# Optimization experiments

Hardware: AMD Instinct MI355X
Metric: run time of the kernel (lower is better)

The kernel has to match this reference:

```python
import jax, jax.numpy as jnp
import numpy as np

B, T, F = 64, 512, 256
ENC = 256      # encoder output dim
P = 128        # projection_dim
H = 256        # gru_hidden_dim
K = 12         # num_future_steps
TEMP = 0.1


def setup_inputs() -> dict:
    key = jax.random.key(0)
    ks = jax.random.split(key, 12)
    s = lambda *d: 1.0 / np.sqrt(d[0])
    return {
        "x_seq": jax.random.normal(ks[0], (B, T, F), jnp.float32),
        # encoder: Dense(F -> ENC)
        "W_enc": jax.random.normal(ks[1], (F, ENC), jnp.float32) * s(F),
        "b_enc": jnp.zeros((ENC,), jnp.float32),
        # projection: Dense(ENC -> P)
        "W_proj": jax.random.normal(ks[2], (ENC, P), jnp.float32) * s(ENC),
        "b_proj": jnp.zeros((P,), jnp.float32),
        # GRUCell (flax convention: input dense has bias, hidden dense bias only on n)
        "Wi": jax.random.normal(ks[3], (P, 3 * H), jnp.float32) * s(P),
        "bi": jnp.zeros((3 * H,), jnp.float32),
        "Wh": jax.random.normal(ks[4], (H, 3 * H), jnp.float32) * s(H),
        "bhn": jnp.zeros((H,), jnp.float32),
        # K predictors: Dense(H -> P)
        "Wp": jax.random.normal(ks[5], (K, H, P), jnp.float32) * s(H),
        "bp": jnp.zeros((K, P), jnp.float32),
    }


def _gru_scan(z_seq, Wi, bi, Wh, bhn):
    # z_seq: [B, T, P] -> c_seq: [B, T, H]
    def step(h, x_t):
        gi = x_t @ Wi + bi          # [B, 3H]
        gh = h @ Wh                 # [B, 3H]
        ir, iz, inn = jnp.split(gi, 3, axis=-1)
        hr, hz, hn = jnp.split(gh, 3, axis=-1)
        r = jax.nn.sigmoid(ir + hr)
        z = jax.nn.sigmoid(iz + hz)
        n = jnp.tanh(inn + r * (hn + bhn))
        h_new = (1.0 - z) * n + z * h
        return h_new, h_new

    h0 = jnp.zeros((z_seq.shape[0], Wh.shape[0]), z_seq.dtype)
    _, c = jax.lax.scan(step, h0, jnp.swapaxes(z_seq, 0, 1))  # c: [T, B, H]
    return jnp.swapaxes(c, 0, 1)


def reference(x_seq, W_enc, b_enc, W_proj, b_proj, Wi, bi, Wh, bhn, Wp, bp):
    # encoder per timestep (vmap(vmap(Dense)) == batched matmul)
    z_seq = x_seq @ W_enc + b_enc                 # [B, T, ENC]
    z_seq = z_seq @ W_proj + b_proj               # [B, T, P]
    c_seq = _gru_scan(z_seq, Wi, bi, Wh, bhn)     # [B, T, H]

    Tlen = z_seq.shape[1]
    loss = jnp.asarray(0.0, z_seq.dtype)
    for k in range(1, K + 1):
        if Tlen - k <= 0:
            continue
        z_pos = z_seq[:, k:]                      # [B, T-k, P]
        pred = c_seq[:, :-k] @ Wp[k - 1] + bp[k - 1]  # [B, T-k, P]
        logits = jnp.einsum('btd,bkd->btk', pred, z_pos) / TEMP
        labels = jnp.arange(logits.shape[1])
        # NOTE: faithful to source: [..., labels] with labels=arange is an
        # identity gather along the last axis (not a diagonal pick).
        loss = loss + jnp.mean(-jax.nn.log_softmax(logits, axis=-1)[..., labels])
    return loss / K
```

## Files before the change

kernel.cpp:

```cpp
#include <hip/hip_runtime.h>
#include <hip/hip_bf16.h>
#include <math.h>

#define B_   64
#define T_   512
#define F_   256
#define ENC_ 256
#define P_   128
#define H_   256
#define K_   12
#define INV_TEMP 10.0f

typedef unsigned short u16;
typedef _Float16 half2v __attribute__((ext_vector_type(2)));
union U2H { unsigned int u; half2v h; };
typedef __attribute__((ext_vector_type(8))) short bf16x8;
typedef __attribute__((ext_vector_type(4))) float f32x4;
typedef _Float16 f16x8 __attribute__((ext_vector_type(8)));
union BF8 { bf16x8 v; u16 e[8]; };

__device__ __forceinline__ float rcpf(float x) {
#if __has_builtin(__builtin_amdgcn_rcpf)
    return __builtin_amdgcn_rcpf(x);
#else
    return 1.f / x;
#endif
}
__device__ __forceinline__ u16 f2bf(float f) {
    unsigned int u = __float_as_uint(f);
    unsigned int r = (u + 0x7fffu + ((u >> 16) & 1u)) >> 16;
    return (u16)r;
}
__device__ __forceinline__ float bf2f(u16 v) {
    return __uint_as_float(((unsigned int)v) << 16);
}
__device__ __forceinline__ float bflo(unsigned int u) { return __uint_as_float(u << 16); }
__device__ __forceinline__ float bfhi(unsigned int u) { return __uint_as_float(u & 0xffff0000u); }
__device__ __forceinline__ float wave_sum(float v) {
    #pragma unroll
    for (int o = 32; o > 0; o >>= 1) v += __shfl_down(v, o, 64);
    return v;
}

__global__ __launch_bounds__(256) void setup_conv(const float* __restrict__ Wh,
                                                  _Float16* __restrict__ Wht,
                                                  const float* __restrict__ Wi,
                                                  u16* __restrict__ Wit,
                                                  const float* __restrict__ Wp,
                                                  u16* __restrict__ Wpt,
                                                  const float* __restrict__ We,
                                                  const float* __restrict__ be,
                                                  const float* __restrict__ Wpj,
                                                  const float* __restrict__ bpj,
                                                  u16* __restrict__ Wct,
                                                  float* __restrict__ bc,
                                                  float* __restrict__ accum) {
    int bid = blockIdx.x;
    if (bid < 192) {
        __shared__ float tile0[32][33];
        int g0 = (bid % 24) * 32, k0 = (bid / 24) * 32;
        int tx = threadIdx.x & 31, ty = threadIdx.x >> 5;
        #pragma unroll
        for (int i = 0; i < 32; i += 8)
            tile0[ty + i][tx] = Wh[(size_t)(k0 + ty + i) * 768 + g0 + tx];
        __syncthreads();
        #pragma unroll
        for (int i = 0; i < 32; i += 8)
            Wht[(size_t)(g0 + ty + i) * 256 + k0 + tx] = (_Float16)tile0[tx][ty + i];
    } else if (bid < 288) {
        __shared__ float tile[32][33];
        int b2 = bid - 192;
        int n0 = (b2 % 24) * 32, k0 = (b2 / 24) * 32;
        int tx = threadIdx.x & 31, ty = threadIdx.x >> 5;
        #pragma unroll
        for (int i = 0; i < 32; i += 8)
            tile[ty + i][tx] = Wi[(size_t)(k0 + ty + i) * 768 + n0 + tx];
        __syncthreads();
        #pragma unroll
        for (int i = 0; i < 32; i += 8)
            Wit[(size_t)(n0 + ty + i) * 128 + k0 + tx] = f2bf(tile[tx][ty + i]);
    } else if (bid < 672) {
        __shared__ float tile2[32][33];
        int b3 = bid - 288;
        int kq = b3 / 32, rem = b3 % 32;
        int h0 = (rem % 8) * 32, p0 = (rem / 8) * 32;
        int tx = threadIdx.x & 31, ty = threadIdx.x >> 5;
        #pragma unroll
        for (int i = 0; i < 32; i += 8)
            tile2[ty + i][tx] = Wp[(size_t)kq * H_ * P_ + (size_t)(h0 + ty + i) * P_ + p0 + tx];
        __syncthreads();
        #pragma unroll
        for (int i = 0; i < 32; i += 8)
            Wpt[(size_t)kq * P_ * H_ + (size_t)(p0 + ty + i) * H_ + h0 + tx] = f2bf(tile2[tx][ty + i]);
    } else {
        int f = (bid - 672) * 2 + (threadIdx.x >> 7);
        int p = threadIdx.x & 127;
        if (f < F_) {
            float a = 0.f;
            for (int e = 0; e < ENC_; e++) a = fmaf(We[f * ENC_ + e], Wpj[e * P_ + p], a);
            Wct[(size_t)p * F_ + f] = f2bf(a);
        } else if (f == F_) {
            float a = bpj[p];
            for (int e = 0; e < ENC_; e++) a = fmaf(be[e], Wpj[e * P_ + p], a);
            bc[p] = a;
        } else {
            #pragma unroll
            for (int i = 0; i < 8; i++) accum[p * 8 + i] = 0.f;
        }
    }
}

__global__ __launch_bounds__(256) void gemm_mfma_f32a(const float* __restrict__ A,
                                                      const u16* __restrict__ Bt,
                                                      const float* __restrict__ bias,
                                                      u16* __restrict__ Ch,
                                                      int N, int K) {
    int tid  = threadIdx.x;
    int w    = tid >> 6;
    int lane = tid & 63;
    int col  = lane & 15;
    int quad = lane >> 4;
    int bm = blockIdx.y * 64, bn = blockIdx.x * 128;

    f32x4 acc[8] = {};
    const float* arow = A + (size_t)(bm + w * 16 + col) * K;
    #pragma unroll
    for (int k0 = 0; k0 < K; k0 += 32) {
        float4 v0 = *(const float4*)(arow + k0 + quad * 8);
        float4 v1 = *(const float4*)(arow + k0 + quad * 8 + 4);
        BF8 af;
        af.e[0] = f2bf(v0.x); af.e[1] = f2bf(v0.y); af.e[2] = f2bf(v0.z); af.e[3] = f2bf(v0.w);
        af.e[4] = f2bf(v1.x); af.e[5] = f2bf(v1.y); af.e[6] = f2bf(v1.z); af.e[7] = f2bf(v1.w);
        #pragma unroll
        for (int nt = 0; nt < 8; nt++) {
            bf16x8 bf = *(const bf16x8*)(Bt + (size_t)(bn + nt * 16 + col) * K + k0 + quad * 8);
            acc[nt] = __builtin_amdgcn_mfma_f32_16x16x32_bf16(af.v, bf, acc[nt], 0, 0, 0);
        }
    }
    #pragma unroll
    for (int nt = 0; nt < 8; nt++) {
        int gn = bn + nt * 16 + col;
        float bv = bias[gn];
        #pragma unroll
        for (int r = 0; r < 4; r++) {
            int gm = bm + w * 16 + quad * 4 + r;
            Ch[(size_t)gm * N + gn] = f2bf(acc[nt][r] + bv);
        }
    }
}

__global__ __launch_bounds__(256) void gemm_mfma(const u16* __restrict__ A,
                                                 const u16* __restrict__ Bt,
                                                 const float* __restrict__ bias,
                                                 u16* __restrict__ Ch,
                                                 int N, int K) {
    int tid  = threadIdx.x;
    int w    = tid >> 6;
    int lane = tid & 63;
    int col  = lane & 15;
    int quad = lane >> 4;
    int bm = blockIdx.y * 64, bn = blockIdx.x * 128;

    f32x4 acc[8] = {};
    const u16* arow = A + (size_t)(bm + w * 16 + col) * K;
    #pragma unroll
    for (int k0 = 0; k0 < K; k0 += 32) {
        bf16x8 af = *(const bf16x8*)(arow + k0 + quad * 8);
        #pragma unroll
        for (int nt = 0; nt < 8; nt++) {
            bf16x8 bf = *(const bf16x8*)(Bt + (size_t)(bn + nt * 16 + col) * K + k0 + quad * 8);
            acc[nt] = __builtin_amdgcn_mfma_f32_16x16x32_bf16(af, bf, acc[nt], 0, 0, 0);
        }
    }
    #pragma unroll
    for (int nt = 0; nt < 8; nt++) {
        int gn = bn + nt * 16 + col;
        float bv = bias[gn];
        #pragma unroll
        for (int r = 0; r < 4; r++) {
            int gm = bm + w * 16 + quad * 4 + r;
            Ch[(size_t)gm * N + gn] = f2bf(acc[nt][r] + bv);
        }
    }
}

#define GRUB_ 64

__global__ __attribute__((amdgpu_flat_work_group_size(512, 512)))
void gru_zsum_kernel(const u16* __restrict__ gi,
                     const _Float16* __restrict__ Wht,
                     const float* __restrict__ bhn,
                     u16* __restrict__ ch,
                     const u16* __restrict__ zh,
                     float* __restrict__ zsum) {
    __shared__ __align__(16) char smem[8704];
    int tid = threadIdx.x;

    if (blockIdx.x >= GRUB_) {
        float (*part)[128] = (float (*)[128])smem;
        int b   = blockIdx.x - GRUB_;
        int pg  = tid & 31;
        int g   = tid >> 5;
        const u16* zb = zh + (size_t)b * T_ * P_;
        float s0 = 0.f, s1 = 0.f, s2 = 0.f, s3 = 0.f;
        for (int t = 1 + g; t < T_; t += 16) {
            uint2 v = *(const uint2*)(zb + (size_t)t * P_ + pg * 4);
            s0 += bflo(v.x); s1 += bfhi(v.x);
            s2 += bflo(v.y); s3 += bfhi(v.y);
        }
        part[g][pg * 4 + 0] = s0; part[g][pg * 4 + 1] = s1;
        part[g][pg * 4 + 2] = s2; part[g][pg * 4 + 3] = s3;
        __syncthreads();
        if (tid < 128) {
            float s = 0.f;
            #pragma unroll
            for (int g2 = 0; g2 < 16; g2++) s += part[g2][tid];
            zsum[(size_t)b * P_ + tid] = s;
        }
        return;
    }

    _Float16* hbase = (_Float16*)smem;

    int lane = tid & 63, w = tid >> 6;
    int col  = lane & 15, quad = lane >> 4;
    int b    = blockIdx.x;
    int jj0  = w * 32 + col;

    f16x8 wf[3][2][8];
    #pragma unroll
    for (int g = 0; g < 3; g++)
        #pragma unroll
        for (int n2 = 0; n2 < 2; n2++) {
            const _Float16* src = Wht + (size_t)(g * 256 + jj0 + n2 * 16) * 256 + quad * 8;
            #pragma unroll
            for (int k0 = 0; k0 < 8; k0++)
                wf[g][n2][k0] = *(const f16x8*)(src + k0 * 32);
        }
    #pragma unroll
    for (int g = 0; g < 3; g++)
        #pragma unroll
        for (int n2 = 0; n2 < 2; n2++)
            #pragma unroll
            for (int k0 = 0; k0 < 8; k0++)
                asm volatile("" : "+v"(wf[g][n2][k0]));

    for (int i = tid; i < 528; i += 512) hbase[i] = (_Float16)0.f;

    const u16* gb = gi + (size_t)b * T_ * 768;
    u16* cb       = ch + (size_t)b * T_ * 256;
    float bh0 = bhn[jj0], bh1 = bhn[jj0 + 16];
    float hold0 = 0.f, hold1 = 0.f;
    unsigned int pf[2][6];

    {
        pf[0][0] = gb[jj0];        pf[0][1] = gb[jj0 + 16];
        pf[0][2] = gb[256 + jj0];  pf[0][3] = gb[256 + jj0 + 16];
        pf[0][4] = gb[512 + jj0];  pf[0][5] = gb[512 + jj0 + 16];
    }
    __syncthreads();

    auto body = [&](int t, int c, int pt) {
        int n = c ^ 1;
        if (pt < T_) {
            const u16* gr = gb + (size_t)pt * 768;
            pf[n][0] = gr[jj0];        pf[n][1] = gr[jj0 + 16];
            pf[n][2] = gr[256 + jj0];  pf[n][3] = gr[256 + jj0 + 16];
            pf[n][4] = gr[512 + jj0];  pf[n][5] = gr[512 + jj0 + 16];
        }
        const _Float16* HC = hbase + c * 264;
        _Float16*       HN = hbase + n * 264;
        f32x4 aR0 = {}, aR1 = {}, aZ0 = {}, aZ1 = {}, aN0 = {}, aN1 = {};
        #pragma unroll
        for (int k0 = 0; k0 < 8; k0++) {
            f16x8 af = *(const f16x8*)(HC + k0 * 32 + quad * 8);
            aR0 = __builtin_amdgcn_mfma_f32_16x16x32_f16(af, wf[0][0][k0], aR0, 0, 0, 0);
            aR1 = __builtin_amdgcn_mfma_f32_16x16x32_f16(af, wf[0][1][k0], aR1, 0, 0, 0);
            aZ0 = __builtin_amdgcn_mfma_f32_16x16x32_f16(af, wf[1][0][k0], aZ0, 0, 0, 0);
            aZ1 = __builtin_amdgcn_mfma_f32_16x16x32_f16(af, wf[1][1][k0], aZ1, 0, 0, 0);
            aN0 = __builtin_amdgcn_mfma_f32_16x16x32_f16(af, wf[2][0][k0], aN0, 0, 0, 0);
            aN1 = __builtin_amdgcn_mfma_f32_16x16x32_f16(af, wf[2][1][k0], aN1, 0, 0, 0);
        }
        float rg0 = rcpf(1.f + __expf(-(bf2f((u16)pf[c][0]) + aR0[0])));
        float rg1 = rcpf(1.f + __expf(-(bf2f((u16)pf[c][1]) + aR1[0])));
        float zg0 = rcpf(1.f + __expf(-(bf2f((u16)pf[c][2]) + aZ0[0])));
        float zg1 = rcpf(1.f + __expf(-(bf2f((u16)pf[c][3]) + aZ1[0])));
        float xn0 = bf2f((u16)pf[c][4]) + rg0 * (aN0[0] + bh0);
        float xn1 = bf2f((u16)pf[c][5]) + rg1 * (aN1[0] + bh1);
        float nn0 = fmaf(2.f, rcpf(1.f + __expf(-2.f * xn0)), -1.f);
        float nn1 = fmaf(2.f, rcpf(1.f + __expf(-2.f * xn1)), -1.f);
        hold0 = (1.f - zg0) * nn0 + zg0 * hold0;
        hold1 = (1.f - zg1) * nn1 + zg1 * hold1;
        if (quad == 0) {
            HN[jj0]      = (_Float16)hold0;
            HN[jj0 + 16] = (_Float16)hold1;
        } else if (quad == 1) {
            u16* cr = cb + (size_t)t * 256;
            cr[jj0]      = f2bf(hold0);
            cr[jj0 + 16] = f2bf(hold1);
        }
        asm volatile("s_waitcnt lgkmcnt(0)" ::: "memory");
        __builtin_amdgcn_s_barrier();
        asm volatile("" ::: "memory");
    };

    #pragma unroll 1
    for (int t = 0; t < T_; t += 2) {
        body(t,     0, t + 1);
        body(t + 1, 1, t + 2);
    }
}

__global__ __launch_bounds__(512) void loss_fused(const u16* __restrict__ ch,
                                                  const u16* __restrict__ Wpt,
                                                  const float* __restrict__ bp,
                                                  const u16* __restrict__ zh,
                                                  const float* __restrict__ zsum,
                                                  float* __restrict__ accum) {
    __shared__ u16 Pst[128][136];
    __shared__ u16 Zt[64][136];
    __shared__ float sS[128];
    __shared__ float red[8];
    int k  = blockIdx.z + 1;
    int b  = blockIdx.y;
    int t0 = blockIdx.x * 128;
    int Tk = T_ - k;
    int tid  = threadIdx.x;
    int w    = tid >> 6;
    int lane = tid & 63;
    int col  = lane & 15;
    int quad = lane >> 4;
    const u16* zb = zh + (size_t)b * T_ * P_;

    if (tid < 128) {
        float s = zsum[(size_t)b * P_ + tid];
        for (int t = 1; t < k; t++) s -= bf2f(zb[(size_t)t * P_ + tid]);
        sS[tid] = s;
    }

    {
        f32x4 acc[8] = {};
        const u16* arow = ch + ((size_t)b * T_ + t0 + w * 16 + col) * H_;
        const u16* wk   = Wpt + (size_t)(k - 1) * P_ * H_;
        #pragma unroll
        for (int k0 = 0; k0 < 8; k0++) {
            bf16x8 af = *(const bf16x8*)(arow + k0 * 32 + quad * 8);
            #pragma unroll
            for (int nt = 0; nt < 8; nt++) {
                bf16x8 bf = *(const bf16x8*)(wk + (size_t)(nt * 16 + col) * H_ + k0 * 32 + quad * 8);
                acc[nt] = __builtin_amdgcn_mfma_f32_16x16x32_bf16(af, bf, acc[nt], 0, 0, 0);
            }
        }
        #pragma unroll
        for (int nt = 0; nt < 8; nt++) {
            float bias = bp[(size_t)(k - 1) * P_ + nt * 16 + col];
            #pragma unroll
            for (int r = 0; r < 4; r++)
                Pst[w * 16 + quad * 4 + r][nt * 16 + col] = f2bf(acc[nt][r] + bias);
        }
    }
    __syncthreads();

    float mloc[4], sloc[4];
    #pragma unroll
    for (int r = 0; r < 4; r++) { mloc[r] = -INFINITY; sloc[r] = 0.f; }

    for (int ct = 0; ct < Tk; ct += 64) {
        __syncthreads();
        {
            int cc = tid;
            #pragma unroll
            for (int rep = 0; rep < 2; rep++, cc += 512) {
                int row = cc >> 4;
                int off = (cc & 15) * 8;
                int tcol = k + ct + row;
                *(uint4*)&Zt[row][off] = *(const uint4*)(zb + (size_t)tcol * P_ + off);
            }
        }
        __syncthreads();
        f32x4 acc[4] = {};
        #pragma unroll
        for (int k0 = 0; k0 < 4; k0++) {
            bf16x8 af = *(const bf16x8*)(&Pst[w * 16 + col][k0 * 32 + quad * 8]);
            #pragma unroll
            for (int nt = 0; nt < 4; nt++) {
                bf16x8 bf = *(const bf16x8*)(&Zt[nt * 16 + col][k0 * 32 + quad * 8]);
                acc[nt] = __builtin_amdgcn_mfma_f32_16x16x32_bf16(af, bf, acc[nt], 0, 0, 0);
            }
        }
        #pragma unroll
        for (int r = 0; r < 4; r++) {
            float l[4];
            float tmax = -INFINITY;
            #pragma unroll
            for (int nt = 0; nt < 4; nt++) {
                bool valid = (ct + nt * 16 + col) < Tk;
                l[nt] = valid ? acc[nt][r] * INV_TEMP : -INFINITY;
                tmax = fmaxf(tmax, l[nt]);
            }
            float mnew = fmaxf(mloc[r], tmax);
            float e = __expf(l[0] - mnew) + __expf(l[1] - mnew)
                    + __expf(l[2] - mnew) + __expf(l[3] - mnew);
            sloc[r] = sloc[r] * __expf(mloc[r] - mnew) + e;
            mloc[r] = mnew;
        }
    }
    #pragma unroll
    for (int r = 0; r < 4; r++) {
        #pragma unroll
        for (int o = 1; o < 16; o <<= 1) {
            float mo = __shfl_xor(mloc[r], o, 64);
            float so = __shfl_xor(sloc[r], o, 64);
            float mn = fmaxf(mloc[r], mo);
            sloc[r] = sloc[r] * __expf(mloc[r] - mn) + so * __expf(mo - mn);
            mloc[r] = mn;
        }
    }
    float tkinv = INV_TEMP / (float)Tk;
    float scale = 1.0f / ((float)K_ * (float)B_ * (float)Tk);
    float bs = 0.f;
    #pragma unroll
    for (int r = 0; r < 4; r++) {
        int row = w * 16 + quad * 4 + r;
        BF8 pv;
        pv.v = *(const bf16x8*)(&Pst[row][col * 8]);
        float d = 0.f;
        #pragma unroll
        for (int m = 0; m < 8; m++) d = fmaf(bf2f(pv.e[m]), sS[col * 8 + m], d);
        #pragma unroll
        for (int o = 1; o < 16; o <<= 1) d += __shfl_xor(d, o, 64);
        int gr = t0 + row;
        if (gr < Tk) bs += mloc[r] + __logf(sloc[r]) - d * tkinv;
    }
    if (col != 0) bs = 0.f;
    bs = wave_sum(bs);
    if (lane == 0) red[w] = bs;
    __syncthreads();
    if (tid == 0) {
        float tot = 0.f;
        #pragma unroll
        for (int i = 0; i < 8; i++) tot += red[i];
        atomicAdd(&accum[(blockIdx.x * 809 + b * 67 + blockIdx.z * 131) & 1023],
                  tot * scale);
    }
}

__global__ void finalize(const float* __restrict__ accum, float* __restrict__ out) {
    int tid = threadIdx.x;
    __shared__ float red[4];
    float v = 0.f;
    for (int i = tid; i < 1024; i += 256) v += accum[i];
    float sres = wave_sum(v);
    if ((tid & 63) == 0) red[tid >> 6] = sres;
    __syncthreads();
    if (tid == 0) out[0] = red[0] + red[1] + red[2] + red[3];
}

extern "C" void kernel_launch(void* const* d_in, const int* in_sizes, int n_in,
                              void* d_out, int out_size, void* d_ws, size_t ws_size,
                              hipStream_t stream) {
    const float* x      = (const float*)d_in[0];
    const float* W_enc  = (const float*)d_in[1];
    const float* b_enc  = (const float*)d_in[2];
    const float* W_proj = (const float*)d_in[3];
    const float* b_proj = (const float*)d_in[4];
    const float* Wi     = (const float*)d_in[5];
    const float* bi     = (const float*)d_in[6];
    const float* Wh     = (const float*)d_in[7];
    const float* bhn    = (const float*)d_in[8];
    const float* Wp     = (const float*)d_in[9];
    const float* bp     = (const float*)d_in[10];
    float* out = (float*)d_out;

    float* ws    = (float*)d_ws;
    float* bc    = ws;
    float* accum = bc + 128;
    _Float16* Wht = (_Float16*)(ws + 1152);
    u16* Wct     = (u16*)(ws + 99456);
    u16* Wit     = (u16*)(ws + 115840);
    u16* Wpt     = (u16*)(ws + 164992);
    u16* zh      = (u16*)(ws + 361600);
    float* zsum  = ws + 2458752;
    u16* gi      = (u16*)(ws + 2466944);
    u16* ch      = (u16*)(ws + 15049856);

    const int MT = B_ * T_;

    setup_conv<<<801, 256, 0, stream>>>(Wh, Wht, Wi, Wit, Wp, Wpt,
                                        W_enc, b_enc, W_proj, b_proj, Wct, bc, accum);
    gemm_mfma_f32a<<<dim3(1, MT / 64), 256, 0, stream>>>(x, Wct, bc, zh, P_, F_);
    gemm_mfma<<<dim3(6, MT / 64), 256, 0, stream>>>(zh, Wit, bi, gi, 3 * H_, P_);
    gru_zsum_kernel<<<GRUB_ + B_, 512, 0, stream>>>(gi, Wht, bhn, ch, zh, zsum);
    loss_fused<<<dim3(4, B_, K_), 512, 0, stream>>>(ch, Wpt, bp, zh, zsum, accum);
    finalize<<<1, 256, 0, stream>>>(accum, out);
}
```

Measured before the change: 953.6 us.

## Split GRU recurrent matmul between MFMA and packed fp16 dot2 VALU paths

Each GRU timestep's hidden-state matmul is split in two. The first half of K (128) still goes through the MFMA chain, and the second half is computed with packed fp16 dot2 instructions on the vector ALU, reduced across quads with lane shuffles. Weights for both halves stay resident in registers. The aim is to shorten the serial MFMA dependency chain per step by running VALU work alongside it, at the cost of more registers, extra shuffles and VALU pressure. The gate-input prefetch is also changed from a double-buffered load one step ahead to a single-buffered load issued at the end of each step.

```diff
diff --git a/kernel.cpp b/kernel.cpp
--- a/kernel.cpp
+++ b/kernel.cpp
@@ -19,6 +19,14 @@
 typedef _Float16 f16x8 __attribute__((ext_vector_type(8)));
 union BF8 { bf16x8 v; u16 e[8]; };
 
+__device__ __forceinline__ float dot2f16(unsigned int a, unsigned int b, float c) {
+    U2H ua; ua.u = a; U2H ub; ub.u = b;
+#if __has_builtin(__builtin_amdgcn_fdot2)
+    return __builtin_amdgcn_fdot2(ua.h, ub.h, c, false);
+#else
+    return fmaf((float)ua.h.x, (float)ub.h.x, fmaf((float)ua.h.y, (float)ub.h.y, c));
+#endif
+}
 __device__ __forceinline__ float rcpf(float x) {
 #if __has_builtin(__builtin_amdgcn_rcpf)
     return __builtin_amdgcn_rcpf(x);
@@ -185,6 +193,8 @@
 }
 
 #define GRUB_ 64
+#define K1_   128
+#define KT1_  4
 
 __global__ __attribute__((amdgpu_flat_work_group_size(512, 512)))
 void gru_zsum_kernel(const u16* __restrict__ gi,
@@ -227,23 +237,37 @@
     int b    = blockIdx.x;
     int jj0  = w * 32 + col;
 
-    f16x8 wf[3][2][8];
+    f16x8 wf[3][2][KT1_];
     #pragma unroll
     for (int g = 0; g < 3; g++)
         #pragma unroll
         for (int n2 = 0; n2 < 2; n2++) {
             const _Float16* src = Wht + (size_t)(g * 256 + jj0 + n2 * 16) * 256 + quad * 8;
             #pragma unroll
-            for (int k0 = 0; k0 < 8; k0++)
+            for (int k0 = 0; k0 < KT1_; k0++)
                 wf[g][n2][k0] = *(const f16x8*)(src + k0 * 32);
         }
+    unsigned int dw[3][2][16];
     #pragma unroll
     for (int g = 0; g < 3; g++)
         #pragma unroll
-        for (int n2 = 0; n2 < 2; n2++)
-            #pragma unroll
-            for (int k0 = 0; k0 < 8; k0++)
+        for (int n2 = 0; n2 < 2; n2++) {
+            const unsigned int* wsrc = (const unsigned int*)
+                (Wht + (size_t)(g * 256 + jj0 + n2 * 16) * 256 + K1_ + quad * 32);
+            #pragma unroll
+            for (int i = 0; i < 16; i++) dw[g][n2][i] = wsrc[i];
+        }
+    #pragma unroll
+    for (int g = 0; g < 3; g++)
+        #pragma unroll
+        for (int n2 = 0; n2 < 2; n2++) {
+            #pragma unroll
+            for (int k0 = 0; k0 < KT1_; k0++)
                 asm volatile("" : "+v"(wf[g][n2][k0]));
+            #pragma unroll
+            for (int i = 0; i < 16; i++)
+                asm volatile("" : "+v"(dw[g][n2][i]));
+        }
 
     for (int i = tid; i < 528; i += 512) hbase[i] = (_Float16)0.f;
 
@@ -251,28 +275,22 @@
     u16* cb       = ch + (size_t)b * T_ * 256;
     float bh0 = bhn[jj0], bh1 = bhn[jj0 + 16];
     float hold0 = 0.f, hold1 = 0.f;
-    unsigned int pf[2][6];
+    unsigned int pf[6];
 
     {
-        pf[0][0] = gb[jj0];        pf[0][1] = gb[jj0 + 16];
-        pf[0][2] = gb[256 + jj0];  pf[0][3] = gb[256 + jj0 + 16];
-        pf[0][4] = gb[512 + jj0];  pf[0][5] = gb[512 + jj0 + 16];
+        pf[0] = gb[jj0];        pf[1] = gb[jj0 + 16];
+        pf[2] = gb[256 + jj0];  pf[3] = gb[256 + jj0 + 16];
+        pf[4] = gb[512 + jj0];  pf[5] = gb[512 + jj0 + 16];
     }
     __syncthreads();
 
-    auto body = [&](int t, int c, int pt) {
+    auto body = [&](int t, int c) {
         int n = c ^ 1;
-        if (pt < T_) {
-            const u16* gr = gb + (size_t)pt * 768;
-            pf[n][0] = gr[jj0];        pf[n][1] = gr[jj0 + 16];
-            pf[n][2] = gr[256 + jj0];  pf[n][3] = gr[256 + jj0 + 16];
-            pf[n][4] = gr[512 + jj0];  pf[n][5] = gr[512 + jj0 + 16];
-        }
         const _Float16* HC = hbase + c * 264;
         _Float16*       HN = hbase + n * 264;
         f32x4 aR0 = {}, aR1 = {}, aZ0 = {}, aZ1 = {}, aN0 = {}, aN1 = {};
         #pragma unroll
-        for (int k0 = 0; k0 < 8; k0++) {
+        for (int k0 = 0; k0 < KT1_; k0++) {
             f16x8 af = *(const f16x8*)(HC + k0 * 32 + quad * 8);
             aR0 = __builtin_amdgcn_mfma_f32_16x16x32_f16(af, wf[0][0][k0], aR0, 0, 0, 0);
             aR1 = __builtin_amdgcn_mfma_f32_16x16x32_f16(af, wf[0][1][k0], aR1, 0, 0, 0);
@@ -281,12 +299,48 @@
             aN0 = __builtin_amdgcn_mfma_f32_16x16x32_f16(af, wf[2][0][k0], aN0, 0, 0, 0);
             aN1 = __builtin_amdgcn_mfma_f32_16x16x32_f16(af, wf[2][1][k0], aN1, 0, 0, 0);
         }
-        float rg0 = rcpf(1.f + __expf(-(bf2f((u16)pf[c][0]) + aR0[0])));
-        float rg1 = rcpf(1.f + __expf(-(bf2f((u16)pf[c][1]) + aR1[0])));
-        float zg0 = rcpf(1.f + __expf(-(bf2f((u16)pf[c][2]) + aZ0[0])));
-        float zg1 = rcpf(1.f + __expf(-(bf2f((u16)pf[c][3]) + aZ1[0])));
-        float xn0 = bf2f((u16)pf[c][4]) + rg0 * (aN0[0] + bh0);
-        float xn1 = bf2f((u16)pf[c][5]) + rg1 * (aN1[0] + bh1);
+        float pR0 = 0.f, pR1 = 0.f, pZ0 = 0.f, pZ1 = 0.f, pN0 = 0.f, pN1 = 0.f;
+        const uint4* hp = (const uint4*)(HC + K1_ + quad * 32);
+        #pragma unroll
+        for (int cc = 0; cc < 4; cc++) {
+            uint4 hv = hp[cc];
+            pR0 = dot2f16(hv.x, dw[0][0][cc*4+0], pR0);
+            pR0 = dot2f16(hv.y, dw[0][0][cc*4+1], pR0);
+            pR0 = dot2f16(hv.z, dw[0][0][cc*4+2], pR0);
+            pR0 = dot2f16(hv.w, dw[0][0][cc*4+3], pR0);
+            pR1 = dot2f16(hv.x, dw[0][1][cc*4+0], pR1);
+            pR1 = dot2f16(hv.y, dw[0][1][cc*4+1], pR1);
+            pR1 = dot2f16(hv.z, dw[0][1][cc*4+2], pR1);
+            pR1 = dot2f16(hv.w, dw[0][1][cc*4+3], pR1);
+            pZ0 = dot2f16(hv.x, dw[1][0][cc*4+0], pZ0);
+            pZ0 = dot2f16(hv.y, dw[1][0][cc*4+1], pZ0);
+            pZ0 = dot2f16(hv.z, dw[1][0][cc*4+2], pZ0);
+            pZ0 = dot2f16(hv.w, dw[1][0][cc*4+3], pZ0);
+            pZ1 = dot2f16(hv.x, dw[1][1][cc*4+0], pZ1);
+            pZ1 = dot2f16(hv.y, dw[1][1][cc*4+1], pZ1);
+            pZ1 = dot2f16(hv.z, dw[1][1][cc*4+2], pZ1);
+            pZ1 = dot2f16(hv.w, dw[1][1][cc*4+3], pZ1);
+            pN0 = dot2f16(hv.x, dw[2][0][cc*4+0], pN0);
+            pN0 = dot2f16(hv.y, dw[2][0][cc*4+1], pN0);
+            pN0 = dot2f16(hv.z, dw[2][0][cc*4+2], pN0);
+            pN0 = dot2f16(hv.w, dw[2][0][cc*4+3], pN0);
+            pN1 = dot2f16(hv.x, dw[2][1][cc*4+0], pN1);
+            pN1 = dot2f16(hv.y, dw[2][1][cc*4+1], pN1);
+            pN1 = dot2f16(hv.z, dw[2][1][cc*4+2], pN1);
+            pN1 = dot2f16(hv.w, dw[2][1][cc*4+3], pN1);
+        }
+        pR0 += __shfl_xor(pR0, 16, 64); pR0 += __shfl_xor(pR0, 32, 64);
+        pR1 += __shfl_xor(pR1, 16, 64); pR1 += __shfl_xor(pR1, 32, 64);
+        pZ0 += __shfl_xor(pZ0, 16, 64); pZ0 += __shfl_xor(pZ0, 32, 64);
+        pZ1 += __shfl_xor(pZ1, 16, 64); pZ1 += __shfl_xor(pZ1, 32, 64);
+        pN0 += __shfl_xor(pN0, 16, 64); pN0 += __shfl_xor(pN0, 32, 64);
+        pN1 += __shfl_xor(pN1, 16, 64); pN1 += __shfl_xor(pN1, 32, 64);
+        float rg0 = rcpf(1.f + __expf(-(bf2f((u16)pf[0]) + aR0[0] + pR0)));
+        float rg1 = rcpf(1.f + __expf(-(bf2f((u16)pf[1]) + aR1[0] + pR1)));
+        float zg0 = rcpf(1.f + __expf(-(bf2f((u16)pf[2]) + aZ0[0] + pZ0)));
+        float zg1 = rcpf(1.f + __expf(-(bf2f((u16)pf[3]) + aZ1[0] + pZ1)));
+        float xn0 = bf2f((u16)pf[4]) + rg0 * (aN0[0] + pN0 + bh0);
+        float xn1 = bf2f((u16)pf[5]) + rg1 * (aN1[0] + pN1 + bh1);
         float nn0 = fmaf(2.f, rcpf(1.f + __expf(-2.f * xn0)), -1.f);
         float nn1 = fmaf(2.f, rcpf(1.f + __expf(-2.f * xn1)), -1.f);
         hold0 = (1.f - zg0) * nn0 + zg0 * hold0;
@@ -299,6 +353,12 @@
             cr[jj0]      = f2bf(hold0);
             cr[jj0 + 16] = f2bf(hold1);
         }
+        if (t + 1 < T_) {
+            const u16* gr = gb + (size_t)(t + 1) * 768;
+            pf[0] = gr[jj0];        pf[1] = gr[jj0 + 16];
+            pf[2] = gr[256 + jj0];  pf[3] = gr[256 + jj0 + 16];
+            pf[4] = gr[512 + jj0];  pf[5] = gr[512 + jj0 + 16];
+        }
         asm volatile("s_waitcnt lgkmcnt(0)" ::: "memory");
         __builtin_amdgcn_s_barrier();
         asm volatile("" ::: "memory");
@@ -306,8 +366,8 @@
 
     #pragma unroll 1
     for (int t = 0; t < T_; t += 2) {
-        body(t,     0, t + 1);
-        body(t + 1, 1, t + 2);
+        body(t,     0);
+        body(t + 1, 1);
     }
 }
 
```

After: 1.170 ms. 22.7% more time.

## Fuse GRU scan with loss kernel via persistent work queue and progress flags

Applied to the files above, without the earlier changes.

Merges the GRU recurrence, z-sum, and contrastive loss into one persistent kernel. GRU blocks publish per-batch progress every 128 timesteps, and loss work tiles are pulled from an atomic queue that waits on those flags. This lets loss computation overlap the serial GRU scan instead of running after it, and it also moves the gi prefetch to after the gate math. The cost is spin-waiting, co-residency assumptions for forward progress, and relying on counters in accum being zeroed by setup, with the accumulator range halved to 512.

```diff
diff --git a/kernel.cpp b/kernel.cpp
--- a/kernel.cpp
+++ b/kernel.cpp
@@ -10,6 +10,7 @@
 #define H_   256
 #define K_   12
 #define INV_TEMP 10.0f
+#define NT_  3072
 
 typedef unsigned short u16;
 typedef _Float16 half2v __attribute__((ext_vector_type(2)));
@@ -184,23 +185,123 @@
     }
 }
 
-#define GRUB_ 64
-
 __global__ __attribute__((amdgpu_flat_work_group_size(512, 512)))
-void gru_zsum_kernel(const u16* __restrict__ gi,
-                     const _Float16* __restrict__ Wht,
-                     const float* __restrict__ bhn,
-                     u16* __restrict__ ch,
-                     const u16* __restrict__ zh,
-                     float* __restrict__ zsum) {
-    __shared__ __align__(16) char smem[8704];
-    int tid = threadIdx.x;
-
-    if (blockIdx.x >= GRUB_) {
+void gru_zsum_loss(const u16* __restrict__ gi,
+                   const _Float16* __restrict__ Wht,
+                   const float* __restrict__ bhn,
+                   u16* __restrict__ ch,
+                   const u16* __restrict__ zh,
+                   float* __restrict__ zsum,
+                   const u16* __restrict__ Wpt,
+                   const float* __restrict__ bp,
+                   float* __restrict__ accum) {
+    __shared__ __align__(16) char smem[52804];
+    int tid  = threadIdx.x;
+    int bid  = blockIdx.x;
+    int lane = tid & 63, w = tid >> 6;
+    int col  = lane & 15, quad = lane >> 4;
+    int* progress = (int*)(accum + 512);
+    int* zflagA   = progress + 64;
+    int* qctr     = progress + 128;
+
+    if (bid < 64) {
+        _Float16* hbase = (_Float16*)smem;
+        int b   = bid;
+        int jj0 = w * 32 + col;
+
+        f16x8 wf[3][2][8];
+        #pragma unroll
+        for (int g = 0; g < 3; g++)
+            #pragma unroll
+            for (int n2 = 0; n2 < 2; n2++) {
+                const _Float16* src = Wht + (size_t)(g * 256 + jj0 + n2 * 16) * 256 + quad * 8;
+                #pragma unroll
+                for (int k0 = 0; k0 < 8; k0++)
+                    wf[g][n2][k0] = *(const f16x8*)(src + k0 * 32);
+            }
+        #pragma unroll
+        for (int g = 0; g < 3; g++)
+            #pragma unroll
+            for (int n2 = 0; n2 < 2; n2++)
+                #pragma unroll
+                for (int k0 = 0; k0 < 8; k0++)
+                    asm volatile("" : "+v"(wf[g][n2][k0]));
+
+        for (int i = tid; i < 528; i += 512) hbase[i] = (_Float16)0.f;
+
+        const u16* gb = gi + (size_t)b * T_ * 768;
+        u16* cb       = ch + (size_t)b * T_ * 256;
+        float bh0 = bhn[jj0], bh1 = bhn[jj0 + 16];
+        float hold0 = 0.f, hold1 = 0.f;
+        unsigned int pf[6];
+        pf[0] = gb[jj0];        pf[1] = gb[jj0 + 16];
+        pf[2] = gb[256 + jj0];  pf[3] = gb[256 + jj0 + 16];
+        pf[4] = gb[512 + jj0];  pf[5] = gb[512 + jj0 + 16];
+        __syncthreads();
+
+        auto body = [&](int t, int c) {
+            int n = c ^ 1;
+            const _Float16* HC = hbase + c * 264;
+            _Float16*       HN = hbase + n * 264;
+            f32x4 aR0 = {}, aR1 = {}, aZ0 = {}, aZ1 = {}, aN0 = {}, aN1 = {};
+            #pragma unroll
+            for (int k0 = 0; k0 < 8; k0++) {
+                f16x8 af = *(const f16x8*)(HC + k0 * 32 + quad * 8);
+                aR0 = __builtin_amdgcn_mfma_f32_16x16x32_f16(af, wf[0][0][k0], aR0, 0, 0, 0);
+                aR1 = __builtin_amdgcn_mfma_f32_16x16x32_f16(af, wf[0][1][k0], aR1, 0, 0, 0);
+                aZ0 = __builtin_amdgcn_mfma_f32_16x16x32_f16(af, wf[1][0][k0], aZ0, 0, 0, 0);
+                aZ1 = __builtin_amdgcn_mfma_f32_16x16x32_f16(af, wf[1][1][k0], aZ1, 0, 0, 0);
+                aN0 = __builtin_amdgcn_mfma_f32_16x16x32_f16(af, wf[2][0][k0], aN0, 0, 0, 0);
+                aN1 = __builtin_amdgcn_mfma_f32_16x16x32_f16(af, wf[2][1][k0], aN1, 0, 0, 0);
+            }
+            float rg0 = rcpf(1.f + __expf(-(bf2f((u16)pf[0]) + aR0[0])));
+            float rg1 = rcpf(1.f + __expf(-(bf2f((u16)pf[1]) + aR1[0])));
+            float zg0 = rcpf(1.f + __expf(-(bf2f((u16)pf[2]) + aZ0[0])));
+            float zg1 = rcpf(1.f + __expf(-(bf2f((u16)pf[3]) + aZ1[0])));
+            float xn0 = bf2f((u16)pf[4]) + rg0 * (aN0[0] + bh0);
+            float xn1 = bf2f((u16)pf[5]) + rg1 * (aN1[0] + bh1);
+            float nn0 = fmaf(2.f, rcpf(1.f + __expf(-2.f * xn0)), -1.f);
+            float nn1 = fmaf(2.f, rcpf(1.f + __expf(-2.f * xn1)), -1.f);
+            hold0 = (1.f - zg0) * nn0 + zg0 * hold0;
+            hold1 = (1.f - zg1) * nn1 + zg1 * hold1;
+            if (quad == 0) {
+                HN[jj0]      = (_Float16)hold0;
+                HN[jj0 + 16] = (_Float16)hold1;
+            } else if (quad == 1) {
+                u16* cr = cb + (size_t)t * 256;
+                cr[jj0]      = f2bf(hold0);
+                cr[jj0 + 16] = f2bf(hold1);
+            }
+            if (t + 1 < T_) {
+                const u16* gr = gb + (size_t)(t + 1) * 768;
+                pf[0] = gr[jj0];        pf[1] = gr[jj0 + 16];
+                pf[2] = gr[256 + jj0];  pf[3] = gr[256 + jj0 + 16];
+                pf[4] = gr[512 + jj0];  pf[5] = gr[512 + jj0 + 16];
+            }
+            asm volatile("s_waitcnt lgkmcnt(0)" ::: "memory");
+            __builtin_amdgcn_s_barrier();
+            asm volatile("" ::: "memory");
+        };
+
+        #pragma unroll 1
+        for (int t = 0; t < T_; t += 2) {
+            body(t,     0);
+            body(t + 1, 1);
+            if (((t + 2) & 127) == 0) {
+                asm volatile("s_waitcnt vmcnt(0)" ::: "memory");
+                __syncthreads();
+                if (tid == 0) {
+                    __threadfence();
+                    __hip_atomic_store(progress + b, t + 2,
+                                       __ATOMIC_RELEASE, __HIP_MEMORY_SCOPE_AGENT);
+                }
+            }
+        }
+    } else if (bid < 128) {
         float (*part)[128] = (float (*)[128])smem;
-        int b   = blockIdx.x - GRUB_;
-        int pg  = tid & 31;
-        int g   = tid >> 5;
+        int b  = bid - 64;
+        int pg = tid & 31;
+        int g  = tid >> 5;
         const u16* zb = zh + (size_t)b * T_ * P_;
         float s0 = 0.f, s1 = 0.f, s2 = 0.f, s3 = 0.f;
         for (int t = 1 + g; t < T_; t += 16) {
@@ -217,231 +318,156 @@
             for (int g2 = 0; g2 < 16; g2++) s += part[g2][tid];
             zsum[(size_t)b * P_ + tid] = s;
         }
-        return;
-    }
-
-    _Float16* hbase = (_Float16*)smem;
-
-    int lane = tid & 63, w = tid >> 6;
-    int col  = lane & 15, quad = lane >> 4;
-    int b    = blockIdx.x;
-    int jj0  = w * 32 + col;
-
-    f16x8 wf[3][2][8];
-    #pragma unroll
-    for (int g = 0; g < 3; g++)
-        #pragma unroll
-        for (int n2 = 0; n2 < 2; n2++) {
-            const _Float16* src = Wht + (size_t)(g * 256 + jj0 + n2 * 16) * 256 + quad * 8;
-            #pragma unroll
-            for (int k0 = 0; k0 < 8; k0++)
-                wf[g][n2][k0] = *(const f16x8*)(src + k0 * 32);
-        }
-    #pragma unroll
-    for (int g = 0; g < 3; g++)
-        #pragma unroll
-        for (int n2 = 0; n2 < 2; n2++)
-            #pragma unroll
-            for (int k0 = 0; k0 < 8; k0++)
-                asm volatile("" : "+v"(wf[g][n2][k0]));
-
-    for (int i = tid; i < 528; i += 512) hbase[i] = (_Float16)0.f;
-
-    const u16* gb = gi + (size_t)b * T_ * 768;
-    u16* cb       = ch + (size_t)b * T_ * 256;
-    float bh0 = bhn[jj0], bh1 = bhn[jj0 + 16];
-    float hold0 = 0.f, hold1 = 0.f;
-    unsigned int pf[2][6];
-
-    {
-        pf[0][0] = gb[jj0];        pf[0][1] = gb[jj0 + 16];
-        pf[0][2] = gb[256 + jj0];  pf[0][3] = gb[256 + jj0 + 16];
-        pf[0][4] = gb[512 + jj0];  pf[0][5] = gb[512 + jj0 + 16];
-    }
-    __syncthreads();
-
-    auto body = [&](int t, int c, int pt) {
-        int n = c ^ 1;
-        if (pt < T_) {
-            const u16* gr = gb + (size_t)pt * 768;
-            pf[n][0] = gr[jj0];        pf[n][1] = gr[jj0 + 16];
-            pf[n][2] = gr[256 + jj0];  pf[n][3] = gr[256 + jj0 + 16];
-            pf[n][4] = gr[512 + jj0];  pf[n][5] = gr[512 + jj0 + 16];
-        }
-        const _Float16* HC = hbase + c * 264;
-        _Float16*       HN = hbase + n * 264;
-        f32x4 aR0 = {}, aR1 = {}, aZ0 = {}, aZ1 = {}, aN0 = {}, aN1 = {};
-        #pragma unroll
-        for (int k0 = 0; k0 < 8; k0++) {
-            f16x8 af = *(const f16x8*)(HC + k0 * 32 + quad * 8);
-            aR0 = __builtin_amdgcn_mfma_f32_16x16x32_f16(af, wf[0][0][k0], aR0, 0, 0, 0);
-            aR1 = __builtin_amdgcn_mfma_f32_16x16x32_f16(af, wf[0][1][k0], aR1, 0, 0, 0);
-            aZ0 = __builtin_amdgcn_mfma_f32_16x16x32_f16(af, wf[1][0][k0], aZ0, 0, 0, 0);
-            aZ1 = __builtin_amdgcn_mfma_f32_16x16x32_f16(af, wf[1][1][k0], aZ1, 0, 0, 0);
-            aN0 = __builtin_amdgcn_mfma_f32_16x16x32_f16(af, wf[2][0][k0], aN0, 0, 0, 0);
-            aN1 = __builtin_amdgcn_mfma_f32_16x16x32_f16(af, wf[2][1][k0], aN1, 0, 0, 0);
-        }
-        float rg0 = rcpf(1.f + __expf(-(bf2f((u16)pf[c][0]) + aR0[0])));
-        float rg1 = rcpf(1.f + __expf(-(bf2f((u16)pf[c][1]) + aR1[0])));
-        float zg0 = rcpf(1.f + __expf(-(bf2f((u16)pf[c][2]) + aZ0[0])));
-        float zg1 = rcpf(1.f + __expf(-(bf2f((u16)pf[c][3]) + aZ1[0])));
-        float xn0 = bf2f((u16)pf[c][4]) + rg0 * (aN0[0] + bh0);
-        float xn1 = bf2f((u16)pf[c][5]) + rg1 * (aN1[0] + bh1);
-        float nn0 = fmaf(2.f, rcpf(1.f + __expf(-2.f * xn0)), -1.f);
-        float nn1 = fmaf(2.f, rcpf(1.f + __expf(-2.f * xn1)), -1.f);
-        hold0 = (1.f - zg0) * nn0 + zg0 * hold0;
-        hold1 = (1.f - zg1) * nn1 + zg1 * hold1;
-        if (quad == 0) {
-            HN[jj0]      = (_Float16)hold0;
-            HN[jj0 + 16] = (_Float16)hold1;
-        } else if (quad == 1) {
-            u16* cr = cb + (size_t)t * 256;
-            cr[jj0]      = f2bf(hold0);
-            cr[jj0 + 16] = f2bf(hold1);
-        }
-        asm volatile("s_waitcnt lgkmcnt(0)" ::: "memory");
-        __builtin_amdgcn_s_barrier();
-        asm volatile("" ::: "memory");
-    };
-
-    #pragma unroll 1
-    for (int t = 0; t < T_; t += 2) {
-        body(t,     0, t + 1);
-        body(t + 1, 1, t + 2);
-    }
-}
-
-__global__ __launch_bounds__(512) void loss_fused(const u16* __restrict__ ch,
-                                                  const u16* __restrict__ Wpt,
-                                                  const float* __restrict__ bp,
-                                                  const u16* __restrict__ zh,
-                                                  const float* __restrict__ zsum,
-                                                  float* __restrict__ accum) {
-    __shared__ u16 Pst[128][136];
-    __shared__ u16 Zt[64][136];
-    __shared__ float sS[128];
-    __shared__ float red[8];
-    int k  = blockIdx.z + 1;
-    int b  = blockIdx.y;
-    int t0 = blockIdx.x * 128;
-    int Tk = T_ - k;
-    int tid  = threadIdx.x;
-    int w    = tid >> 6;
-    int lane = tid & 63;
-    int col  = lane & 15;
-    int quad = lane >> 4;
-    const u16* zb = zh + (size_t)b * T_ * P_;
-
-    if (tid < 128) {
-        float s = zsum[(size_t)b * P_ + tid];
-        for (int t = 1; t < k; t++) s -= bf2f(zb[(size_t)t * P_ + tid]);
-        sS[tid] = s;
-    }
-
-    {
-        f32x4 acc[8] = {};
-        const u16* arow = ch + ((size_t)b * T_ + t0 + w * 16 + col) * H_;
-        const u16* wk   = Wpt + (size_t)(k - 1) * P_ * H_;
-        #pragma unroll
-        for (int k0 = 0; k0 < 8; k0++) {
-            bf16x8 af = *(const bf16x8*)(arow + k0 * 32 + quad * 8);
+        asm volatile("s_waitcnt vmcnt(0)" ::: "memory");
+        __syncthreads();
+        if (tid == 0) {
+            __threadfence();
+            __hip_atomic_store(zflagA + b, 1, __ATOMIC_RELEASE, __HIP_MEMORY_SCOPE_AGENT);
+        }
+    }
+
+    u16 (*Pst)[136] = (u16 (*)[136])smem;
+    u16 (*Zt)[136]  = (u16 (*)[136])(smem + 34816);
+    float* sS       = (float*)(smem + 52224);
+    float* red      = (float*)(smem + 52736);
+    int*   sTile    = (int*)(smem + 52768);
+
+    while (true) {
+        if (tid == 0) *sTile = atomicAdd(qctr, 1);
+        __syncthreads();
+        int tile = *sTile;
+        __syncthreads();
+        if (tile >= NT_) break;
+
+        int t0i = tile / 768;
+        int rem = tile - t0i * 768;
+        int b   = rem & 63;
+        int kz  = rem >> 6;
+        int k   = kz + 1;
+        int t0  = t0i * 128;
+        int Tk  = T_ - k;
+        int need = (t0i + 1) << 7;
+        if (tid == 0) {
+            while (__hip_atomic_load(zflagA + b, __ATOMIC_ACQUIRE, __HIP_MEMORY_SCOPE_AGENT) == 0)
+                __builtin_amdgcn_s_sleep(2);
+            while (__hip_atomic_load(progress + b, __ATOMIC_ACQUIRE, __HIP_MEMORY_SCOPE_AGENT) < need)
+                __builtin_amdgcn_s_sleep(2);
+        }
+        __syncthreads();
+
+        const u16* zb = zh + (size_t)b * T_ * P_;
+
+        if (tid < 128) {
+            float s = zsum[(size_t)b * P_ + tid];
+            for (int t = 1; t < k; t++) s -= bf2f(zb[(size_t)t * P_ + tid]);
+            sS[tid] = s;
+        }
+
+        {
+            f32x4 acc[8] = {};
+            const u16* arow = ch + ((size_t)b * T_ + t0 + w * 16 + col) * H_;
+            const u16* wk   = Wpt + (size_t)(k - 1) * P_ * H_;
+            #pragma unroll
+            for (int k0 = 0; k0 < 8; k0++) {
+                bf16x8 af = *(const bf16x8*)(arow + k0 * 32 + quad * 8);
+                #pragma unroll
+                for (int nt = 0; nt < 8; nt++) {
+                    bf16x8 bf = *(const bf16x8*)(wk + (size_t)(nt * 16 + col) * H_ + k0 * 32 + quad * 8);
+                    acc[nt] = __builtin_amdgcn_mfma_f32_16x16x32_bf16(af, bf, acc[nt], 0, 0, 0);
+                }
+            }
             #pragma unroll
             for (int nt = 0; nt < 8; nt++) {
-                bf16x8 bf = *(const bf16x8*)(wk + (size_t)(nt * 16 + col) * H_ + k0 * 32 + quad * 8);
-                acc[nt] = __builtin_amdgcn_mfma_f32_16x16x32_bf16(af, bf, acc[nt], 0, 0, 0);
-            }
-        }
-        #pragma unroll
-        for (int nt = 0; nt < 8; nt++) {
-            float bias = bp[(size_t)(k - 1) * P_ + nt * 16 + col];
-            #pragma unroll
-            for (int r = 0; r < 4; r++)
-                Pst[w * 16 + quad * 4 + r][nt * 16 + col] = f2bf(acc[nt][r] + bias);
-        }
-    }
-    __syncthreads();
-
-    float mloc[4], sloc[4];
-    #pragma unroll
-    for (int r = 0; r < 4; r++) { mloc[r] = -INFINITY; sloc[r] = 0.f; }
-
-    for (int ct = 0; ct < Tk; ct += 64) {
-        __syncthreads();
-        {
-            int cc = tid;
-            #pragma unroll
-            for (int rep = 0; rep < 2; rep++, cc += 512) {
-                int row = cc >> 4;
-                int off = (cc & 15) * 8;
-                int tcol = k + ct + row;
-                *(uint4*)&Zt[row][off] = *(const uint4*)(zb + (size_t)tcol * P_ + off);
-            }
-        }
-        __syncthreads();
-        f32x4 acc[4] = {};
-        #pragma unroll
-        for (int k0 = 0; k0 < 4; k0++) {
-            bf16x8 af = *(const bf16x8*)(&Pst[w * 16 + col][k0 * 32 + quad * 8]);
-            #pragma unroll
-            for (int nt = 0; nt < 4; nt++) {
-                bf16x8 bf = *(const bf16x8*)(&Zt[nt * 16 + col][k0 * 32 + quad * 8]);
-                acc[nt] = __builtin_amdgcn_mfma_f32_16x16x32_bf16(af, bf, acc[nt], 0, 0, 0);
+                float bias = bp[(size_t)(k - 1) * P_ + nt * 16 + col];
+                #pragma unroll
+                for (int r = 0; r < 4; r++)
+                    Pst[w * 16 + quad * 4 + r][nt * 16 + col] = f2bf(acc[nt][r] + bias);
+            }
+        }
+        __syncthreads();
+
+        float mloc[4], sloc[4];
+        #pragma unroll
+        for (int r = 0; r < 4; r++) { mloc[r] = -INFINITY; sloc[r] = 0.f; }
+
+        for (int ct = 0; ct < Tk; ct += 64) {
+            __syncthreads();
+            {
+                int cc = tid;
+                #pragma unroll
+                for (int rep = 0; rep < 2; rep++, cc += 512) {
+                    int row = cc >> 4;
+                    int off = (cc & 15) * 8;
+                    int tcol = k + ct + row;
+                    *(uint4*)&Zt[row][off] = *(const uint4*)(zb + (size_t)tcol * P_ + off);
+                }
+            }
+            __syncthreads();
+            f32x4 acc[4] = {};
+            #pragma unroll
+            for (int k0 = 0; k0 < 4; k0++) {
+                bf16x8 af = *(const bf16x8*)(&Pst[w * 16 + col][k0 * 32 + quad * 8]);
+                #pragma unroll
+                for (int nt = 0; nt < 4; nt++) {
+                    bf16x8 bf = *(const bf16x8*)(&Zt[nt * 16 + col][k0 * 32 + quad * 8]);
+                    acc[nt] = __builtin_amdgcn_mfma_f32_16x16x32_bf16(af, bf, acc[nt], 0, 0, 0);
+                }
+            }
+            #pragma unroll
+            for (int r = 0; r < 4; r++) {
+                float l[4];
+                float tmax = -INFINITY;
+                #pragma unroll
+                for (int nt = 0; nt < 4; nt++) {
+                    bool valid = (ct + nt * 16 + col) < Tk;
+                    l[nt] = valid ? acc[nt][r] * INV_TEMP : -INFINITY;
+                    tmax = fmaxf(tmax, l[nt]);
+                }
+                float mnew = fmaxf(mloc[r], tmax);
+                float e = __expf(l[0] - mnew) + __expf(l[1] - mnew)
+                        + __expf(l[2] - mnew) + __expf(l[3] - mnew);
+                sloc[r] = sloc[r] * __expf(mloc[r] - mnew) + e;
+                mloc[r] = mnew;
             }
         }
         #pragma unroll
         for (int r = 0; r < 4; r++) {
-            float l[4];
-            float tmax = -INFINITY;
-            #pragma unroll
-            for (int nt = 0; nt < 4; nt++) {
-                bool valid = (ct + nt * 16 + col) < Tk;
-                l[nt] = valid ? acc[nt][r] * INV_TEMP : -INFINITY;
-                tmax = fmaxf(tmax, l[nt]);
-            }
-            float mnew = fmaxf(mloc[r], tmax);
-            float e = __expf(l[0] - mnew) + __expf(l[1] - mnew)
-                    + __expf(l[2] - mnew) + __expf(l[3] - mnew);
-            sloc[r] = sloc[r] * __expf(mloc[r] - mnew) + e;
-            mloc[r] = mnew;
-        }
-    }
-    #pragma unroll
-    for (int r = 0; r < 4; r++) {
-        #pragma unroll
-        for (int o = 1; o < 16; o <<= 1) {
-            float mo = __shfl_xor(mloc[r], o, 64);
-            float so = __shfl_xor(sloc[r], o, 64);
-            float mn = fmaxf(mloc[r], mo);
-            sloc[r] = sloc[r] * __expf(mloc[r] - mn) + so * __expf(mo - mn);
-            mloc[r] = mn;
-        }
-    }
-    float tkinv = INV_TEMP / (float)Tk;
-    float scale = 1.0f / ((float)K_ * (float)B_ * (float)Tk);
-    float bs = 0.f;
-    #pragma unroll
-    for (int r = 0; r < 4; r++) {
-        int row = w * 16 + quad * 4 + r;
-        BF8 pv;
-        pv.v = *(const bf16x8*)(&Pst[row][col * 8]);
-        float d = 0.f;
-        #pragma unroll
-        for (int m = 0; m < 8; m++) d = fmaf(bf2f(pv.e[m]), sS[col * 8 + m], d);
-        #pragma unroll
-        for (int o = 1; o < 16; o <<= 1) d += __shfl_xor(d, o, 64);
-        int gr = t0 + row;
-        if (gr < Tk) bs += mloc[r] + __logf(sloc[r]) - d * tkinv;
-    }
-    if (col != 0) bs = 0.f;
-    bs = wave_sum(bs);
-    if (lane == 0) red[w] = bs;
-    __syncthreads();
-    if (tid == 0) {
-        float tot = 0.f;
-        #pragma unroll
-        for (int i = 0; i < 8; i++) tot += red[i];
-        atomicAdd(&accum[(blockIdx.x * 809 + b * 67 + blockIdx.z * 131) & 1023],
-                  tot * scale);
+            #pragma unroll
+            for (int o = 1; o < 16; o <<= 1) {
+                float mo = __shfl_xor(mloc[r], o, 64);
+                float so = __shfl_xor(sloc[r], o, 64);
+                float mn = fmaxf(mloc[r], mo);
+                sloc[r] = sloc[r] * __expf(mloc[r] - mn) + so * __expf(mo - mn);
+                mloc[r] = mn;
+            }
+        }
+        float tkinv = INV_TEMP / (float)Tk;
+        float scale = 1.0f / ((float)K_ * (float)B_ * (float)Tk);
+        float bs = 0.f;
+        #pragma unroll
+        for (int r = 0; r < 4; r++) {
+            int row = w * 16 + quad * 4 + r;
+            BF8 pv;
+            pv.v = *(const bf16x8*)(&Pst[row][col * 8]);
+            float d = 0.f;
+            #pragma unroll
+            for (int m = 0; m < 8; m++) d = fmaf(bf2f(pv.e[m]), sS[col * 8 + m], d);
+            #pragma unroll
+            for (int o = 1; o < 16; o <<= 1) d += __shfl_xor(d, o, 64);
+            int gr = t0 + row;
+            if (gr < Tk) bs += mloc[r] + __logf(sloc[r]) - d * tkinv;
+        }
+        if (col != 0) bs = 0.f;
+        bs = wave_sum(bs);
+        if (lane == 0) red[w] = bs;
+        __syncthreads();
+        if (tid == 0) {
+            float tot = 0.f;
+            #pragma unroll
+            for (int i = 0; i < 8; i++) tot += red[i];
+            atomicAdd(&accum[(t0i * 809 + b * 67 + kz * 131) & 511], tot * scale);
+        }
+        __syncthreads();
     }
 }
 
@@ -449,7 +475,7 @@
     int tid = threadIdx.x;
     __shared__ float red[4];
     float v = 0.f;
-    for (int i = tid; i < 1024; i += 256) v += accum[i];
+    for (int i = tid; i < 512; i += 256) v += accum[i];
     float sres = wave_sum(v);
     if ((tid & 63) == 0) red[tid >> 6] = sres;
     __syncthreads();
@@ -490,7 +516,6 @@
                                         W_enc, b_enc, W_proj, b_proj, Wct, bc, accum);
     gemm_mfma_f32a<<<dim3(1, MT / 64), 256, 0, stream>>>(x, Wct, bc, zh, P_, F_);
     gemm_mfma<<<dim3(6, MT / 64), 256, 0, stream>>>(zh, Wit, bi, gi, 3 * H_, P_);
-    gru_zsum_kernel<<<GRUB_ + B_, 512, 0, stream>>>(gi, Wht, bhn, ch, zh, zsum);
-    loss_fused<<<dim3(4, B_, K_), 512, 0, stream>>>(ch, Wpt, bp, zh, zsum, accum);
+    gru_zsum_loss<<<256, 512, 0, stream>>>(gi, Wht, bhn, ch, zh, zsum, Wpt, bp, accum);
     finalize<<<1, 256, 0, stream>>>(accum, out);
 }
```

New measurement: 990.1 us. 3.8% more time.
